# Performance work log

Hardware: AMD Instinct MI355X
Metric: run time of the kernel (lower is better)

## Reference

```python
import jax, jax.numpy as jnp
import numpy as np

N_NODES = 500_000
N_EDGES = 16_000_000
N_TYPES = 64


def setup_inputs() -> dict:
    key = jax.random.key(0)
    ks = jax.random.split(key, 8)
    voltage = jax.random.normal(ks[0], (N_NODES,), dtype=jnp.float32)
    stimulus = jax.random.normal(ks[1], (N_NODES,), dtype=jnp.float32)
    neuron_type = jax.random.randint(ks[2], (N_NODES,), 0, N_TYPES, dtype=jnp.int64)
    edge_index = jax.random.randint(ks[3], (2, N_EDGES), 0, N_NODES, dtype=jnp.int64)
    w = jax.random.normal(ks[4], (N_EDGES,), dtype=jnp.float32)
    V_i_rest = jax.random.normal(ks[5], (N_NODES,), dtype=jnp.float32)
    # tau must be positive (divisor); shift uniform away from zero
    tau_i = jax.random.uniform(ks[6], (N_NODES,), dtype=jnp.float32) + 0.5
    # multiple_ReLU per-type scale, abs(1 + 0.5*randn) as in the module
    type_params = jnp.abs(1.0 + 0.5 * jax.random.normal(ks[7], (N_TYPES, 1), dtype=jnp.float32))
    return {
        "voltage": voltage,
        "stimulus": stimulus,
        "neuron_type": neuron_type,
        "edge_index": edge_index,
        "w": w,
        "V_i_rest": V_i_rest,
        "tau_i": tau_i,
        "type_params": type_params,
    }


def reference(voltage, stimulus, neuron_type, edge_index, w, V_i_rest, tau_i, type_params):
    # voltage: (N,), edge_index: (2,E), w: (E,), type_params: (T,1)
    v = voltage[:, None]  # (N,1)
    src = edge_index[0]
    dst = edge_index[1]
    # per-edge message: w_e * relu(v_src) * param[type(src)]   -> (E,1)
    edge_msg = w[:, None] * jax.nn.relu(v[src]) * type_params[neuron_type[src]]
    # scatter_add to destination nodes -> (N,1)
    msg = jax.ops.segment_sum(edge_msg, dst, num_segments=v.shape[0])
    # dv/dt = (-v + msg + e + v_rest) / tau
    dv = (-v + msg + stimulus[:, None] + V_i_rest[:, None]) / tau_i[:, None]
    return dv
```

## Files before the change

kernel.cpp:

```cpp
#include <hip/hip_runtime.h>


#define BSHIFT 9
#define BSIZE  512
#define NBMAX  1024
#define GPB    4096
#define EPB    (GPB * 4)


__global__ void pre_g_kernel(const float* __restrict__ v,
                             const int* __restrict__ ntype,
                             const float* __restrict__ tp,
                             float* __restrict__ g, int n) {
    int i = blockIdx.x * blockDim.x + threadIdx.x;
    if (i < n) {
        float x = v[i];
        x = x > 0.0f ? x : 0.0f;
        g[i] = x * tp[ntype[i]];
    }
}

__global__ void hist_kernel(const int* __restrict__ dst,
                            unsigned* __restrict__ cnt,
                            int G, int n_edges, int nblk, int nb) {
    __shared__ unsigned hist[NBMAX];
    int blk = blockIdx.x, tid = threadIdx.x;
    for (int i = tid; i < NBMAX; i += 512) hist[i] = 0;
    __syncthreads();
    const int4* d4 = (const int4*)dst;
    int gstart = blk * GPB;
    int gend = gstart + GPB; if (gend > G) gend = G;
    for (int i = gstart + tid; i < gend; i += 512) {
        int4 d = d4[i];
        atomicAdd(&hist[((unsigned)d.x) >> BSHIFT], 1u);
        atomicAdd(&hist[((unsigned)d.y) >> BSHIFT], 1u);
        atomicAdd(&hist[((unsigned)d.z) >> BSHIFT], 1u);
        atomicAdd(&hist[((unsigned)d.w) >> BSHIFT], 1u);
    }
    if (blk == nblk - 1) {
        for (int i = G * 4 + tid; i < n_edges; i += 512)
            atomicAdd(&hist[((unsigned)dst[i]) >> BSHIFT], 1u);
    }
    __syncthreads();
    for (int b = tid; b < nb; b += 512)
        cnt[(size_t)blk * nb + b] = hist[b];
}

__global__ void scan_blocks_kernel(unsigned* __restrict__ cnt,
                                   unsigned* __restrict__ total,
                                   int nblk, int nb) {
    __shared__ unsigned buf[256];
    __shared__ unsigned carry;
    int b = blockIdx.x, tid = threadIdx.x;
    if (tid == 0) carry = 0;
    __syncthreads();
    for (int i0 = 0; i0 < nblk; i0 += 256) {
        int i = i0 + tid;
        unsigned v = (i < nblk) ? cnt[(size_t)i * nb + b] : 0u;
        buf[tid] = v;
        __syncthreads();
        for (int o = 1; o < 256; o <<= 1) {
            unsigned t = (tid >= o) ? buf[tid - o] : 0u;
            __syncthreads();
            buf[tid] += t;
            __syncthreads();
        }
        unsigned excl = buf[tid] - v;
        if (i < nblk) cnt[(size_t)i * nb + b] = carry + excl;
        __syncthreads();
        if (tid == 255) carry += buf[255];
        __syncthreads();
    }
    if (tid == 0) total[b] = carry;
}

__global__ void scan_buckets_kernel(const unsigned* __restrict__ total,
                                    unsigned* __restrict__ base, int nb) {
    __shared__ unsigned buf[256];
    int tid = threadIdx.x;
    unsigned v[4];
    unsigned s = 0;
    for (int k = 0; k < 4; k++) {
        int i = tid * 4 + k;
        v[k] = (i < nb) ? total[i] : 0u;
        s += v[k];
    }
    buf[tid] = s;
    __syncthreads();
    for (int o = 1; o < 256; o <<= 1) {
        unsigned t = (tid >= o) ? buf[tid - o] : 0u;
        __syncthreads();
        buf[tid] += t;
        __syncthreads();
    }
    unsigned run = buf[tid] - s;
    for (int k = 0; k < 4; k++) {
        int i = tid * 4 + k;
        if (i < nb) base[i] = run;
        run += v[k];
    }
}

__global__ __launch_bounds__(1024, 8)
void scatter_kernel(const int* __restrict__ src,
                    const int* __restrict__ dst,
                    const float* __restrict__ w,
                    const float* __restrict__ g,
                    const unsigned* __restrict__ base,
                    const unsigned* __restrict__ cnt,
                    const unsigned* __restrict__ total,
                    unsigned* __restrict__ sorted,
                    int G, int n_edges, int nblk, int nb) {
    __shared__ unsigned stage[EPB];
    __shared__ unsigned lcur[NBMAX];
    __shared__ unsigned gseg[NBMAX];
    int blk = blockIdx.x, tid = threadIdx.x;
    bool last = (blk == nblk - 1);

    unsigned cntv = 0;
    if (tid < nb) {
        unsigned pref = cnt[(size_t)blk * nb + tid];
        unsigned nxt  = (blk + 1 < nblk) ? cnt[(size_t)(blk + 1) * nb + tid]
                                         : total[tid];
        cntv = nxt - pref;
        gseg[tid] = base[tid] + pref;
    }
    lcur[tid] = cntv;
    __syncthreads();
    for (int o = 1; o < 1024; o <<= 1) {
        unsigned t = (tid >= o) ? lcur[tid - o] : 0u;
        __syncthreads();
        lcur[tid] += t;
        __syncthreads();
    }
    lcur[tid] -= cntv;
    __syncthreads();

    const int4*   s4 = (const int4*)src;
    const int4*   d4 = (const int4*)dst;
    const float4* w4 = (const float4*)w;
    int gstart = blk * GPB;
    int gend = gstart + GPB; if (gend > G) gend = G;
    for (int i = gstart + tid; i < gend; i += 1024) {
        int4 s = s4[i]; int4 d = d4[i]; float4 wv = w4[i];
        {
            unsigned b = ((unsigned)d.x) >> BSHIFT;
            unsigned pos = atomicAdd(&lcur[b], 1u);
            stage[pos] = (__float_as_uint(wv.x * g[s.x]) & ~(unsigned)(BSIZE - 1)) |
                         ((unsigned)d.x & (BSIZE - 1));
        }
        {
            unsigned b = ((unsigned)d.y) >> BSHIFT;
            unsigned pos = atomicAdd(&lcur[b], 1u);
            stage[pos] = (__float_as_uint(wv.y * g[s.y]) & ~(unsigned)(BSIZE - 1)) |
                         ((unsigned)d.y & (BSIZE - 1));
        }
        {
            unsigned b = ((unsigned)d.z) >> BSHIFT;
            unsigned pos = atomicAdd(&lcur[b], 1u);
            stage[pos] = (__float_as_uint(wv.z * g[s.z]) & ~(unsigned)(BSIZE - 1)) |
                         ((unsigned)d.z & (BSIZE - 1));
        }
        {
            unsigned b = ((unsigned)d.w) >> BSHIFT;
            unsigned pos = atomicAdd(&lcur[b], 1u);
            stage[pos] = (__float_as_uint(wv.w * g[s.w]) & ~(unsigned)(BSIZE - 1)) |
                         ((unsigned)d.w & (BSIZE - 1));
        }
    }
    if (last) {
        for (int i = G * 4 + tid; i < n_edges; i += 1024) {
            int dd = dst[i];
            unsigned b = ((unsigned)dd) >> BSHIFT;
            unsigned pos = atomicAdd(&lcur[b], 1u);
            stage[pos] = (__float_as_uint(w[i] * g[src[i]]) & ~(unsigned)(BSIZE - 1)) |
                         ((unsigned)dd & (BSIZE - 1));
        }
    }
    __syncthreads();

    int wave = tid >> 6, lane = tid & 63;
    for (int b = wave; b < nb; b += 16) {
        unsigned lend = lcur[b];
        unsigned lstart = (b == 0) ? 0u : lcur[b - 1];
        unsigned gs = gseg[b];
        for (unsigned j = lane; j < lend - lstart; j += 64)
            sorted[gs + j] = stage[lstart + j];
    }
}

__global__ void accum_kernel(const unsigned* __restrict__ sorted,
                             const unsigned* __restrict__ base,
                             const unsigned* __restrict__ total,
                             const float* __restrict__ v,
                             const float* __restrict__ stim,
                             const float* __restrict__ vrest,
                             const float* __restrict__ tau,
                             float* __restrict__ out,
                             int n_nodes) {
    __shared__ float acc[BSIZE];
    int b = blockIdx.x, tid = threadIdx.x;
    acc[tid] = 0.0f;
    __syncthreads();
    unsigned start = base[b], n = total[b];
    for (unsigned e = start + tid; e < start + n; e += 512) {
        unsigned u = sorted[e];
        atomicAdd(&acc[u & (BSIZE - 1)],
                  __uint_as_float(u & ~(unsigned)(BSIZE - 1)));
    }
    __syncthreads();
    int i = (b << BSHIFT) + tid;
    if (i < n_nodes)
        out[i] = (-v[i] + acc[tid] + stim[i] + vrest[i]) / tau[i];
}


__global__ void node_pre_kernel(const float* __restrict__ v,
                                const int* __restrict__ ntype,
                                const float* __restrict__ tp,
                                float* __restrict__ g,
                                float* __restrict__ msg, int n) {
    int i = blockIdx.x * blockDim.x + threadIdx.x;
    if (i < n) {
        float x = v[i];
        x = x > 0.0f ? x : 0.0f;
        g[i] = x * tp[ntype[i]];
        msg[i] = 0.0f;
    }
}

__global__ void edge_scatter_kernel(const int* __restrict__ src,
                                    const int* __restrict__ dst,
                                    const float* __restrict__ w,
                                    const float* __restrict__ g,
                                    float* __restrict__ msg, int n_vec) {
    int i = blockIdx.x * blockDim.x + threadIdx.x;
    if (i < n_vec) {
        int4 s = ((const int4*)src)[i];
        int4 d = ((const int4*)dst)[i];
        float4 wv = ((const float4*)w)[i];
        atomicAdd(&msg[d.x], wv.x * g[s.x]);
        atomicAdd(&msg[d.y], wv.y * g[s.y]);
        atomicAdd(&msg[d.z], wv.z * g[s.z]);
        atomicAdd(&msg[d.w], wv.w * g[s.w]);
    }
}

__global__ void edge_scatter_tail(const int* __restrict__ src,
                                  const int* __restrict__ dst,
                                  const float* __restrict__ w,
                                  const float* __restrict__ g,
                                  float* __restrict__ msg,
                                  int start, int n_edges) {
    int i = start + blockIdx.x * blockDim.x + threadIdx.x;
    if (i < n_edges) atomicAdd(&msg[dst[i]], w[i] * g[src[i]]);
}

__global__ void node_post_kernel(const float* __restrict__ v,
                                 const float* __restrict__ msg,
                                 const float* __restrict__ stim,
                                 const float* __restrict__ vrest,
                                 const float* __restrict__ tau,
                                 float* __restrict__ out, int n) {
    int i = blockIdx.x * blockDim.x + threadIdx.x;
    if (i < n)
        out[i] = (-v[i] + msg[i] + stim[i] + vrest[i]) / tau[i];
}


extern "C" void kernel_launch(void* const* d_in, const int* in_sizes, int n_in,
                              void* d_out, int out_size, void* d_ws, size_t ws_size,
                              hipStream_t stream) {
    const float* voltage  = (const float*)d_in[0];
    const float* stimulus = (const float*)d_in[1];
    const int*   ntype    = (const int*)d_in[2];
    const int*   edge_idx = (const int*)d_in[3];
    const float* w        = (const float*)d_in[4];
    const float* vrest    = (const float*)d_in[5];
    const float* tau      = (const float*)d_in[6];
    const float* tp       = (const float*)d_in[7];
    float* out = (float*)d_out;

    const int n_nodes = in_sizes[0];
    const int n_edges = in_sizes[4];
    const int* src = edge_idx;
    const int* dst = edge_idx + n_edges;

    const int B = 256;
    const int G = n_edges / 4;
    int nblk = (G + GPB - 1) / GPB;
    if (nblk < 1) nblk = 1;
    const int nb = (n_nodes + BSIZE - 1) / BSIZE;

    auto align256 = [](size_t x) { return (x + 255) & ~(size_t)255; };
    size_t g_off      = 0;
    size_t sorted_off = align256(g_off + (size_t)n_nodes * 4);
    size_t cnt_off    = align256(sorted_off + (size_t)n_edges * 4);
    size_t total_off  = align256(cnt_off + (size_t)nb * nblk * 4);
    size_t base_off   = align256(total_off + (size_t)nb * 4);
    size_t need       = align256(base_off + (size_t)nb * 4);

    if (nb <= NBMAX && ws_size >= need) {
        float*    g      = (float*)((char*)d_ws + g_off);
        unsigned* sorted = (unsigned*)((char*)d_ws + sorted_off);
        unsigned* cnt    = (unsigned*)((char*)d_ws + cnt_off);
        unsigned* total  = (unsigned*)((char*)d_ws + total_off);
        unsigned* basep  = (unsigned*)((char*)d_ws + base_off);

        pre_g_kernel<<<(n_nodes + B - 1) / B, B, 0, stream>>>(
            voltage, ntype, tp, g, n_nodes);
        hist_kernel<<<nblk, 512, 0, stream>>>(dst, cnt, G, n_edges, nblk, nb);
        scan_blocks_kernel<<<nb, 256, 0, stream>>>(cnt, total, nblk, nb);
        scan_buckets_kernel<<<1, 256, 0, stream>>>(total, basep, nb);
        scatter_kernel<<<nblk, 1024, 0, stream>>>(src, dst, w, g, basep, cnt,
                                                  total, sorted, G, n_edges,
                                                  nblk, nb);
        accum_kernel<<<nb, 512, 0, stream>>>(sorted, basep, total, voltage,
                                             stimulus, vrest, tau, out, n_nodes);
    } else {
        float* g   = (float*)d_ws;
        float* msg = (float*)d_ws + n_nodes;
        node_pre_kernel<<<(n_nodes + B - 1) / B, B, 0, stream>>>(
            voltage, ntype, tp, g, msg, n_nodes);
        if (G > 0)
            edge_scatter_kernel<<<(G + B - 1) / B, B, 0, stream>>>(
                src, dst, w, g, msg, G);
        if (G * 4 < n_edges) {
            int rem = n_edges - G * 4;
            edge_scatter_tail<<<(rem + B - 1) / B, B, 0, stream>>>(
                src, dst, w, g, msg, G * 4, n_edges);
        }
        node_post_kernel<<<(n_nodes + B - 1) / B, B, 0, stream>>>(
            voltage, msg, stimulus, vrest, tau, out, n_nodes);
    }
}
```

Measured before the change: 474.5 us.

## Replace global bucket sort with per-block local sort and segmented accumulation

Removes the separate histogram and the two scan kernels. Each scatter block now counts its own edges into local buckets, scans them in shared memory, and writes its locally sorted stage contiguously, along with a row of per-bucket offsets. The accumulate kernel walks every block's segment for its bucket, so it no longer reads from a globally sorted array. This drops two passes over dst and several launches, but each accumulate thread now handles one block's short segment, about 32 edges, serially. Those reads are uncoalesced, which risks poor memory efficiency in accum.

Result: slower. 517.4 us (+9.1%).

```diff
diff --git a/kernel.cpp b/kernel.cpp
--- a/kernel.cpp
+++ b/kernel.cpp
@@ -20,120 +20,21 @@
     }
 }
 
-__global__ void hist_kernel(const int* __restrict__ dst,
-                            unsigned* __restrict__ cnt,
-                            int G, int n_edges, int nblk, int nb) {
-    __shared__ unsigned hist[NBMAX];
-    int blk = blockIdx.x, tid = threadIdx.x;
-    for (int i = tid; i < NBMAX; i += 512) hist[i] = 0;
-    __syncthreads();
-    const int4* d4 = (const int4*)dst;
-    int gstart = blk * GPB;
-    int gend = gstart + GPB; if (gend > G) gend = G;
-    for (int i = gstart + tid; i < gend; i += 512) {
-        int4 d = d4[i];
-        atomicAdd(&hist[((unsigned)d.x) >> BSHIFT], 1u);
-        atomicAdd(&hist[((unsigned)d.y) >> BSHIFT], 1u);
-        atomicAdd(&hist[((unsigned)d.z) >> BSHIFT], 1u);
-        atomicAdd(&hist[((unsigned)d.w) >> BSHIFT], 1u);
-    }
-    if (blk == nblk - 1) {
-        for (int i = G * 4 + tid; i < n_edges; i += 512)
-            atomicAdd(&hist[((unsigned)dst[i]) >> BSHIFT], 1u);
-    }
-    __syncthreads();
-    for (int b = tid; b < nb; b += 512)
-        cnt[(size_t)blk * nb + b] = hist[b];
-}
-
-__global__ void scan_blocks_kernel(unsigned* __restrict__ cnt,
-                                   unsigned* __restrict__ total,
-                                   int nblk, int nb) {
-    __shared__ unsigned buf[256];
-    __shared__ unsigned carry;
-    int b = blockIdx.x, tid = threadIdx.x;
-    if (tid == 0) carry = 0;
-    __syncthreads();
-    for (int i0 = 0; i0 < nblk; i0 += 256) {
-        int i = i0 + tid;
-        unsigned v = (i < nblk) ? cnt[(size_t)i * nb + b] : 0u;
-        buf[tid] = v;
-        __syncthreads();
-        for (int o = 1; o < 256; o <<= 1) {
-            unsigned t = (tid >= o) ? buf[tid - o] : 0u;
-            __syncthreads();
-            buf[tid] += t;
-            __syncthreads();
-        }
-        unsigned excl = buf[tid] - v;
-        if (i < nblk) cnt[(size_t)i * nb + b] = carry + excl;
-        __syncthreads();
-        if (tid == 255) carry += buf[255];
-        __syncthreads();
-    }
-    if (tid == 0) total[b] = carry;
-}
-
-__global__ void scan_buckets_kernel(const unsigned* __restrict__ total,
-                                    unsigned* __restrict__ base, int nb) {
-    __shared__ unsigned buf[256];
-    int tid = threadIdx.x;
-    unsigned v[4];
-    unsigned s = 0;
-    for (int k = 0; k < 4; k++) {
-        int i = tid * 4 + k;
-        v[k] = (i < nb) ? total[i] : 0u;
-        s += v[k];
-    }
-    buf[tid] = s;
-    __syncthreads();
-    for (int o = 1; o < 256; o <<= 1) {
-        unsigned t = (tid >= o) ? buf[tid - o] : 0u;
-        __syncthreads();
-        buf[tid] += t;
-        __syncthreads();
-    }
-    unsigned run = buf[tid] - s;
-    for (int k = 0; k < 4; k++) {
-        int i = tid * 4 + k;
-        if (i < nb) base[i] = run;
-        run += v[k];
-    }
-}
-
 __global__ __launch_bounds__(1024, 8)
 void scatter_kernel(const int* __restrict__ src,
                     const int* __restrict__ dst,
                     const float* __restrict__ w,
                     const float* __restrict__ g,
-                    const unsigned* __restrict__ base,
-                    const unsigned* __restrict__ cnt,
-                    const unsigned* __restrict__ total,
                     unsigned* __restrict__ sorted,
+                    unsigned* __restrict__ lpref_g,
                     int G, int n_edges, int nblk, int nb) {
     __shared__ unsigned stage[EPB];
+    __shared__ unsigned lstart[NBMAX];
     __shared__ unsigned lcur[NBMAX];
-    __shared__ unsigned gseg[NBMAX];
     int blk = blockIdx.x, tid = threadIdx.x;
     bool last = (blk == nblk - 1);
 
-    unsigned cntv = 0;
-    if (tid < nb) {
-        unsigned pref = cnt[(size_t)blk * nb + tid];
-        unsigned nxt  = (blk + 1 < nblk) ? cnt[(size_t)(blk + 1) * nb + tid]
-                                         : total[tid];
-        cntv = nxt - pref;
-        gseg[tid] = base[tid] + pref;
-    }
-    lcur[tid] = cntv;
-    __syncthreads();
-    for (int o = 1; o < 1024; o <<= 1) {
-        unsigned t = (tid >= o) ? lcur[tid - o] : 0u;
-        __syncthreads();
-        lcur[tid] += t;
-        __syncthreads();
-    }
-    lcur[tid] -= cntv;
+    lcur[tid] = 0;
     __syncthreads();
 
     const int4*   s4 = (const int4*)src;
@@ -141,6 +42,34 @@
     const float4* w4 = (const float4*)w;
     int gstart = blk * GPB;
     int gend = gstart + GPB; if (gend > G) gend = G;
+
+    for (int i = gstart + tid; i < gend; i += 1024) {
+        int4 d = d4[i];
+        atomicAdd(&lcur[((unsigned)d.x) >> BSHIFT], 1u);
+        atomicAdd(&lcur[((unsigned)d.y) >> BSHIFT], 1u);
+        atomicAdd(&lcur[((unsigned)d.z) >> BSHIFT], 1u);
+        atomicAdd(&lcur[((unsigned)d.w) >> BSHIFT], 1u);
+    }
+    if (last) {
+        for (int i = G * 4 + tid; i < n_edges; i += 1024)
+            atomicAdd(&lcur[((unsigned)dst[i]) >> BSHIFT], 1u);
+    }
+    __syncthreads();
+
+    unsigned cntv = lcur[tid];
+    lstart[tid] = cntv;
+    __syncthreads();
+    for (int o = 1; o < 1024; o <<= 1) {
+        unsigned t = (tid >= o) ? lstart[tid - o] : 0u;
+        __syncthreads();
+        lstart[tid] += t;
+        __syncthreads();
+    }
+    unsigned excl = lstart[tid] - cntv;
+    lstart[tid] = excl;
+    lcur[tid] = excl;
+    __syncthreads();
+
     for (int i = gstart + tid; i < gend; i += 1024) {
         int4 s = s4[i]; int4 d = d4[i]; float4 wv = w4[i];
         {
@@ -179,34 +108,39 @@
     }
     __syncthreads();
 
-    int wave = tid >> 6, lane = tid & 63;
-    for (int b = wave; b < nb; b += 16) {
-        unsigned lend = lcur[b];
-        unsigned lstart = (b == 0) ? 0u : lcur[b - 1];
-        unsigned gs = gseg[b];
-        for (unsigned j = lane; j < lend - lstart; j += 64)
-            sorted[gs + j] = stage[lstart + j];
-    }
+    unsigned count = (unsigned)(gend - gstart) * 4u +
+                     (last ? (unsigned)(n_edges - G * 4) : 0u);
+    uint4* out4 = (uint4*)(sorted + (size_t)blk * EPB);
+    const uint4* st4 = (const uint4*)stage;
+    unsigned nq = (count + 3u) >> 2;
+    for (unsigned i = tid; i < nq; i += 1024) out4[i] = st4[i];
+
+    unsigned* row = lpref_g + (size_t)blk * (nb + 1);
+    if (tid < (unsigned)nb)       row[tid] = lstart[tid];
+    else if (tid == (unsigned)nb) row[nb]  = count;
 }
 
 __global__ void accum_kernel(const unsigned* __restrict__ sorted,
-                             const unsigned* __restrict__ base,
-                             const unsigned* __restrict__ total,
+                             const unsigned* __restrict__ lpref_g,
                              const float* __restrict__ v,
                              const float* __restrict__ stim,
                              const float* __restrict__ vrest,
                              const float* __restrict__ tau,
                              float* __restrict__ out,
-                             int n_nodes) {
+                             int n_nodes, int nblk, int nb) {
     __shared__ float acc[BSIZE];
     int b = blockIdx.x, tid = threadIdx.x;
     acc[tid] = 0.0f;
     __syncthreads();
-    unsigned start = base[b], n = total[b];
-    for (unsigned e = start + tid; e < start + n; e += 512) {
-        unsigned u = sorted[e];
-        atomicAdd(&acc[u & (BSIZE - 1)],
-                  __uint_as_float(u & ~(unsigned)(BSIZE - 1)));
+    for (int blk = tid; blk < nblk; blk += 512) {
+        const unsigned* row = lpref_g + (size_t)blk * (nb + 1) + b;
+        unsigned s = row[0], e = row[1];
+        const unsigned* seg = sorted + (size_t)blk * EPB;
+        for (unsigned j = s; j < e; j++) {
+            unsigned u = seg[j];
+            atomicAdd(&acc[u & (BSIZE - 1)],
+                      __uint_as_float(u & ~(unsigned)(BSIZE - 1)));
+        }
     }
     __syncthreads();
     int i = (b << BSHIFT) + tid;
@@ -295,28 +229,21 @@
     auto align256 = [](size_t x) { return (x + 255) & ~(size_t)255; };
     size_t g_off      = 0;
     size_t sorted_off = align256(g_off + (size_t)n_nodes * 4);
-    size_t cnt_off    = align256(sorted_off + (size_t)n_edges * 4);
-    size_t total_off  = align256(cnt_off + (size_t)nb * nblk * 4);
-    size_t base_off   = align256(total_off + (size_t)nb * 4);
-    size_t need       = align256(base_off + (size_t)nb * 4);
-
-    if (nb <= NBMAX && ws_size >= need) {
+    size_t lpref_off  = align256(sorted_off + (size_t)nblk * EPB * 4);
+    size_t need       = align256(lpref_off + (size_t)nblk * (nb + 1) * 4);
+
+    if (nb < NBMAX && ws_size >= need) {
         float*    g      = (float*)((char*)d_ws + g_off);
         unsigned* sorted = (unsigned*)((char*)d_ws + sorted_off);
-        unsigned* cnt    = (unsigned*)((char*)d_ws + cnt_off);
-        unsigned* total  = (unsigned*)((char*)d_ws + total_off);
-        unsigned* basep  = (unsigned*)((char*)d_ws + base_off);
+        unsigned* lpref  = (unsigned*)((char*)d_ws + lpref_off);
 
         pre_g_kernel<<<(n_nodes + B - 1) / B, B, 0, stream>>>(
             voltage, ntype, tp, g, n_nodes);
-        hist_kernel<<<nblk, 512, 0, stream>>>(dst, cnt, G, n_edges, nblk, nb);
-        scan_blocks_kernel<<<nb, 256, 0, stream>>>(cnt, total, nblk, nb);
-        scan_buckets_kernel<<<1, 256, 0, stream>>>(total, basep, nb);
-        scatter_kernel<<<nblk, 1024, 0, stream>>>(src, dst, w, g, basep, cnt,
-                                                  total, sorted, G, n_edges,
-                                                  nblk, nb);
-        accum_kernel<<<nb, 512, 0, stream>>>(sorted, basep, total, voltage,
-                                             stimulus, vrest, tau, out, n_nodes);
+        scatter_kernel<<<nblk, 1024, 0, stream>>>(
+            src, dst, w, g, sorted, lpref, G, n_edges, nblk, nb);
+        accum_kernel<<<nb, 512, 0, stream>>>(
+            sorted, lpref, voltage, stimulus, vrest, tau, out,
+            n_nodes, nblk, nb);
     } else {
         float* g   = (float*)d_ws;
         float* msg = (float*)d_ws + n_nodes;
```
